# Optimization experiments

Measured on AMD Instinct MI355X. Metric: run time of the kernel, lower is better.

The kernel has to match this reference:

```python
import jax, jax.numpy as jnp
import numpy as np

B, NPTS, NBASIS, DIM, H, CH = 8, 1024, 8, 8, 512, 16
EPSILON = 1000.0
P = 2
VOLUME = 2.0 ** DIM  # MC domain [-1,1]^dim


def setup_inputs() -> dict:
    key = jax.random.key(0)
    ks = jax.random.split(key, 10)
    s = jax.random.uniform(ks[0], (NPTS, DIM), dtype=jnp.float32) * 2.0 - 1.0  # MC samples in [-1,1]^dim
    x = jax.random.uniform(ks[1], (1, DIM), dtype=jnp.float32) * 2.0 - 1.0     # eval point
    Wfirst = jax.random.normal(ks[2], (DIM, H), dtype=jnp.float32) / np.sqrt(DIM)
    bfirst = jax.random.normal(ks[3], (H,), dtype=jnp.float32) * 0.01
    Wb = jax.random.normal(ks[4], (NBASIS, H, H), dtype=jnp.float32) / np.sqrt(H)
    bb = jax.random.normal(ks[5], (NBASIS, H), dtype=jnp.float32) * 0.01
    Wlast = jax.random.normal(ks[6], (H, CH), dtype=jnp.float32) / np.sqrt(H)
    blast = jax.random.normal(ks[7], (CH,), dtype=jnp.float32) * 0.01
    Wf = jax.random.normal(ks[8], (DIM, CH), dtype=jnp.float32) / np.sqrt(DIM)
    bf = jax.random.normal(ks[9], (CH,), dtype=jnp.float32) * 0.01
    return dict(s=s, x=x, Wfirst=Wfirst, bfirst=bfirst, Wb=Wb, bb=bb,
                Wlast=Wlast, blast=blast, Wf=Wf, bf=bf)


def _basis_all(pts, Wfirst, bfirst, Wb, bb, Wlast, blast):
    # pts: [M, DIM] -> all n basis nets, batch-repeated: [NBASIS, B, M, CH]
    a0 = jax.nn.elu(jnp.einsum('md,dh->mh', pts, Wfirst) + bfirst)          # [M, H]
    a0 = jnp.broadcast_to(a0[None], (B,) + a0.shape)                         # [B, M, H] (repeat over batch)
    a1 = jax.nn.elu(jnp.einsum('bmh,ihk->ibmk', a0, Wb) + bb[:, None, None, :])  # [n, B, M, H]
    return jnp.einsum('ibmk,kc->ibmc', a1, Wlast) + blast                    # [n, B, M, CH]


def reference(s, x, Wfirst, bfirst, Wb, bb, Wlast, blast, Wf, bf):
    # func(s): linear map realizing the projected function  [NPTS, CH]
    f_s = jnp.einsum('nd,dc->nc', s, Wf) + bf
    basis_s = _basis_all(s, Wfirst, bfirst, Wb, bb, Wlast, blast)            # [n, B, NPTS, CH]
    diff = f_s[None, None] - basis_s                                          # broadcast over n, B
    # Monte Carlo integral of (func - basis_i)^p over [-1,1]^dim, per channel
    integral = VOLUME * jnp.mean(diff ** P, axis=-2)                          # [n, B, CH]
    norm_pc = integral ** (1.0 / P)                                           # Lp norm per channel
    norm_b = jnp.sum(jnp.abs(norm_pc) ** P, axis=-1, keepdims=True) ** (1.0 / P)  # [n, B, 1]
    mu = jnp.where(norm_b <= EPSILON, norm_b, 0.0)                            # [n, B, 1]
    basis_x = _basis_all(x, Wfirst, bfirst, Wb, bb, Wlast, blast)[:, :, 0, :]  # [n, B, CH]
    out = jnp.sum(mu * basis_x, axis=0)                                       # [B, CH]
    normalization = 1e-7 + jnp.sum(mu, axis=0)                                # [B, 1]
    return out / normalization
```

## Files before the change

### kernel.cpp

```cpp
#include <hip/hip_runtime.h>

typedef _Float16 half8 __attribute__((ext_vector_type(8)));
typedef float f32x4 __attribute__((ext_vector_type(4)));
typedef float f32x16 __attribute__((ext_vector_type(16)));
typedef unsigned int u32x4 __attribute__((ext_vector_type(4)));

#define NPTS 1024
#define NB 8
#define HDIM 512
#define CH 16
#define RT 1056

#define OFF_WBF 0u
#define OFF_A0F (4u*1024u*1024u)
#define A0SZ    (64u*RT*16u)
#define OFF_WLF (OFF_A0F + A0SZ)
#define OFF_FS  (OFF_WLF + 16384u)
#define OFF_IS  (OFF_FS + 65536u)
#define OFF_BX  (OFF_IS + 64u)
#define OFF_CT  (OFF_BX + 512u)

__device__ __forceinline__ float elu(float z) { return z > 0.f ? z : expm1f(z); }

__global__ __launch_bounds__(256) void kPrep(const float* __restrict__ s,
    const float* __restrict__ x, const float* __restrict__ Wfirst,
    const float* __restrict__ bfirst, const float* __restrict__ Wb,
    const float* __restrict__ Wlast, const float* __restrict__ Wf,
    const float* __restrict__ bf,
    _Float16* __restrict__ Wbf, _Float16* __restrict__ Wlf,
    _Float16* __restrict__ a0f, float* __restrict__ f_s,
    float* __restrict__ Isum, unsigned* __restrict__ cnt) {
  __shared__ __align__(16) float sm[8192];
  int b = blockIdx.x, t = threadIdx.x;
  if (b < 1024) {
    int i = b >> 7, koct = (b >> 1) & 63, n = (b & 1) * 256 + t;
    const float* src = Wb + ((size_t)i * 512 + koct * 8) * 512 + n;
    float v[8];
#pragma unroll
    for (int j = 0; j < 8; ++j) v[j] = src[j * 512];
    union { _Float16 h[8]; u32x4 u; } hu;
#pragma unroll
    for (int j = 0; j < 8; ++j) hu.h[j] = (_Float16)v[j];
    *(u32x4*)(Wbf + ((size_t)(i * 64 + koct) * 512 + n) * 8) = hu.u;
  } else if (b < 1288) {
    int rr = t >> 6, tl = t & 63;
    int m = (b - 1024) * 4 + rr;
    float* sv = &sm[rr * 8];
    if (tl < 8) sv[tl] = (m < 1024) ? s[m * 8 + tl] : (m == 1024 ? x[tl] : 0.f);
    __syncthreads();
    size_t o = ((size_t)tl * RT + m) * 8;
    if (m <= 1024) {
      float acc[8];
#pragma unroll
      for (int jj = 0; jj < 8; ++jj) acc[jj] = bfirst[8 * tl + jj];
#pragma unroll
      for (int d = 0; d < 8; ++d) {
        float sd = sv[d];
        f32x4 w0 = *(const f32x4*)&Wfirst[d * 512 + 8 * tl];
        f32x4 w1 = *(const f32x4*)&Wfirst[d * 512 + 8 * tl + 4];
#pragma unroll
        for (int e = 0; e < 4; ++e) { acc[e] += sd * w0[e]; acc[4 + e] += sd * w1[e]; }
      }
      union { _Float16 h[8]; u32x4 u; } hu;
#pragma unroll
      for (int jj = 0; jj < 8; ++jj) hu.h[jj] = (_Float16)elu(acc[jj]);
      *(u32x4*)(a0f + o) = hu.u;
      if (m < 1024 && tl < 16) {
        float a = bf[tl];
#pragma unroll
        for (int d = 0; d < 8; ++d) a += sv[d] * Wf[d * 16 + tl];
        f_s[m * 16 + tl] = a;
      }
    } else {
      u32x4 z;
#pragma unroll
      for (int e = 0; e < 4; ++e) z[e] = 0u;
      *(u32x4*)(a0f + o) = z;
    }
  } else {
    if (t < 8) Isum[t] = 0.f;
    if (t == 8) *cnt = 0u;
#pragma unroll
    for (int it = 0; it < 32; ++it) sm[t + 256 * it] = Wlast[t + 256 * it];
    __syncthreads();
#pragma unroll
    for (int p = 0; p < 4; ++p) {
      int oi = p * 256 + t;
      int ko = oi >> 4, ch = oi & 15;
      union { _Float16 h[8]; u32x4 u; } hu;
#pragma unroll
      for (int jj = 0; jj < 8; ++jj) hu.h[jj] = (_Float16)sm[(ko * 8 + jj) * 16 + ch];
      *(u32x4*)(Wlf + oi * 8) = hu.u;
    }
  }
}

__global__ __launch_bounds__(256, 2) void kB(const _Float16* __restrict__ Wbf,
    const _Float16* __restrict__ a0f, const _Float16* __restrict__ Wlf,
    const float* __restrict__ bb, const float* __restrict__ blast,
    const float* __restrict__ f_s, float* __restrict__ Isum,
    float* __restrict__ basisx, unsigned* __restrict__ cnt,
    float* __restrict__ out) {
  __shared__ u32x4 SC[512];
  __shared__ float S2[32][16];
  __shared__ float wsum[4];
  __shared__ unsigned oc;
  __shared__ float muL[8];
  int t = threadIdx.x, b = blockIdx.x;
  int i = b & 7, mt = b >> 3;
  int m0 = mt * 32;
  int w = t >> 6, lane = t & 63, ln = lane & 31, q = lane >> 5, q4 = lane >> 4;

  const u32x4* a4 = (const u32x4*)a0f;
  const u32x4* b4 = (const u32x4*)Wbf;
  int ma = m0 + ln, ib = i * 64;
  int nwl = w * 32 + ln;

  f32x16 acc[4];
#pragma unroll
  for (int j = 0; j < 4; ++j)
#pragma unroll
    for (int rr = 0; rr < 16; ++rr) acc[j][rr] = 0.f;

  u32x4 pa[3][2], pb[3][2][4];
#pragma unroll
  for (int st = 0; st < 2; ++st) {
    int k0 = st * 4 + q, k1 = k0 + 2;
    pa[st][0] = a4[k0 * RT + ma];
    pa[st][1] = a4[k1 * RT + ma];
#pragma unroll
    for (int j = 0; j < 4; ++j) {
      pb[st][0][j] = b4[(size_t)(ib + k0) * 512 + nwl + 128 * j];
      pb[st][1][j] = b4[(size_t)(ib + k1) * 512 + nwl + 128 * j];
    }
  }
#pragma unroll
  for (int ks = 0; ks < 16; ++ks) {
    int sl = ks % 3;
    if (ks < 14) {
      int sn = (ks + 2) % 3;
      int k0 = (ks + 2) * 4 + q, k1 = k0 + 2;
      pa[sn][0] = a4[k0 * RT + ma];
      pa[sn][1] = a4[k1 * RT + ma];
#pragma unroll
      for (int j = 0; j < 4; ++j) {
        pb[sn][0][j] = b4[(size_t)(ib + k0) * 512 + nwl + 128 * j];
        pb[sn][1][j] = b4[(size_t)(ib + k1) * 512 + nwl + 128 * j];
      }
    }
#pragma unroll
    for (int sfx = 0; sfx < 2; ++sfx) {
      half8 aH = __builtin_bit_cast(half8, pa[sl][sfx]);
#pragma unroll
      for (int j = 0; j < 4; ++j)
        acc[j] = __builtin_amdgcn_mfma_f32_32x32x16_f16(
            aH, __builtin_bit_cast(half8, pb[sl][sfx][j]), acc[j], 0, 0, 0);
    }
  }

  ((float*)S2)[t] = 0.f;
  ((float*)S2)[t + 256] = 0.f;
  __syncthreads();

  _Float16* scr = (_Float16*)&SC[w * 128];
  const u32x4* s4 = &SC[w * 128];
  const u32x4* w4 = (const u32x4*)Wlf;
  int ch = lane & 15;
#pragma unroll
  for (int j = 0; j < 4; ++j) {
    int nw = w * 32 + 128 * j;
    float bcol = bb[i * 512 + nw + ln];
#pragma unroll
    for (int rr = 0; rr < 16; ++rr) {
      int row = (rr & 3) + 8 * (rr >> 2) + 4 * q;
      float a1 = elu(acc[j][rr] + bcol);
      int oi = (row >> 4) * 64 + (ln >> 3) * 16 + (row & 15);
      scr[oi * 8 + (ln & 7)] = (_Float16)a1;
    }
    half8 wv = __builtin_bit_cast(half8, w4[(size_t)((nw >> 3) + q4) * 16 + ch]);
#pragma unroll
    for (int mt2 = 0; mt2 < 2; ++mt2) {
      f32x4 D2;
#pragma unroll
      for (int rr = 0; rr < 4; ++rr) D2[rr] = 0.f;
      half8 pv = __builtin_bit_cast(half8, s4[mt2 * 64 + q4 * 16 + ch]);
      D2 = __builtin_amdgcn_mfma_f32_16x16x32_f16(pv, wv, D2, 0, 0, 0);
#pragma unroll
      for (int rr = 0; rr < 4; ++rr)
        atomicAdd(&S2[mt2 * 16 + q4 * 4 + rr][ch], D2[rr]);
    }
  }
  __syncthreads();

  if (mt == 32) {
    if (t < 16) basisx[i * 16 + t] = S2[0][t] + blast[t];
  } else {
    float loc = 0.f;
#pragma unroll
    for (int p = 0; p < 2; ++p) {
      int item = t + p * 256;
      int ml = item >> 4, c2 = item & 15;
      float bs = S2[ml][c2] + blast[c2];
      float d = f_s[(size_t)(m0 + ml) * 16 + c2] - bs;
      loc += d * d;
    }
    loc += __shfl_xor(loc, 1, 64);
    loc += __shfl_xor(loc, 2, 64);
    loc += __shfl_xor(loc, 4, 64);
    loc += __shfl_xor(loc, 8, 64);
    loc += __shfl_xor(loc, 16, 64);
    loc += __shfl_xor(loc, 32, 64);
    if (lane == 0) wsum[w] = loc;
    __syncthreads();
    if (t == 0) atomicAdd(&Isum[i], wsum[0] + wsum[1] + wsum[2] + wsum[3]);
  }

  if (t == 0) {
    __threadfence();
    oc = atomicAdd(cnt, 1u);
  }
  __syncthreads();
  if (oc == 263) {
    __threadfence();
    if (t < 8) {
      float S = atomicAdd(&Isum[t], 0.f);
      float nb = 0.5f * sqrtf(S);
      muL[t] = (nb <= 1000.0f) ? nb : 0.f;
    }
    __syncthreads();
    if (t < 128) {
      int c2 = t & 15;
      float num = 0.f, den = 1e-7f;
#pragma unroll
      for (int ii = 0; ii < NB; ++ii) {
        float bx = atomicAdd(&basisx[ii * 16 + c2], 0.f);
        num += muL[ii] * bx;
        den += muL[ii];
      }
      out[t] = num / den;
    }
  }
}

extern "C" void kernel_launch(void* const* d_in, const int* in_sizes, int n_in,
                              void* d_out, int out_size, void* d_ws, size_t ws_size,
                              hipStream_t stream) {
  const float* s      = (const float*)d_in[0];
  const float* x      = (const float*)d_in[1];
  const float* Wfirst = (const float*)d_in[2];
  const float* bfirst = (const float*)d_in[3];
  const float* Wb     = (const float*)d_in[4];
  const float* bb     = (const float*)d_in[5];
  const float* Wlast  = (const float*)d_in[6];
  const float* blast  = (const float*)d_in[7];
  const float* Wf     = (const float*)d_in[8];
  const float* bf     = (const float*)d_in[9];

  char* ws = (char*)d_ws;
  _Float16* Wbf = (_Float16*)(ws + OFF_WBF);
  _Float16* a0f = (_Float16*)(ws + OFF_A0F);
  _Float16* Wlf = (_Float16*)(ws + OFF_WLF);
  float* f_s    = (float*)(ws + OFF_FS);
  float* Isum   = (float*)(ws + OFF_IS);
  float* basisx = (float*)(ws + OFF_BX);
  unsigned* cnt = (unsigned*)(ws + OFF_CT);
  float* out    = (float*)d_out;

  kPrep<<<1289, 256, 0, stream>>>(s, x, Wfirst, bfirst, Wb, Wlast, Wf, bf,
                                  Wbf, Wlf, a0f, f_s, Isum, cnt);
  kB<<<264, 256, 0, stream>>>(Wbf, a0f, Wlf, bb, blast, f_s, Isum, basisx, cnt, out);
}
```

Measured before the change: 131.2 us.

## Split kB's N dimension across 16 waves per 1024-thread block

The main kernel moves from 256 threads per block, where each wave computed four 32-column tiles, to 1024 threads per block, where each of 16 waves computes a single 32x32 tile. Per-wave accumulator and prefetch register use drops from four f32x16 accumulators to one, and the prefetch pipeline is deepened from three to four stages. The intent is more waves in flight and more latency hiding. In exchange, each wave loads the same A rows independently, shared memory per block grows, and the LDS atomics into S2 now come from 16 waves. The column reduction also fills its scratch before a barrier instead of interleaving with the ELU pass.

```diff
diff --git a/kernel.cpp b/kernel.cpp
--- a/kernel.cpp
+++ b/kernel.cpp
@@ -95,100 +95,85 @@
   }
 }
 
-__global__ __launch_bounds__(256, 2) void kB(const _Float16* __restrict__ Wbf,
+__global__ __launch_bounds__(1024, 4) void kB(const _Float16* __restrict__ Wbf,
     const _Float16* __restrict__ a0f, const _Float16* __restrict__ Wlf,
     const float* __restrict__ bb, const float* __restrict__ blast,
     const float* __restrict__ f_s, float* __restrict__ Isum,
     float* __restrict__ basisx, unsigned* __restrict__ cnt,
     float* __restrict__ out) {
-  __shared__ u32x4 SC[512];
+  __shared__ u32x4 SC[2048];
   __shared__ float S2[32][16];
-  __shared__ float wsum[4];
+  __shared__ float wsum[16];
   __shared__ unsigned oc;
   __shared__ float muL[8];
   int t = threadIdx.x, b = blockIdx.x;
   int i = b & 7, mt = b >> 3;
   int m0 = mt * 32;
   int w = t >> 6, lane = t & 63, ln = lane & 31, q = lane >> 5, q4 = lane >> 4;
+  int nw = w * 32;
 
   const u32x4* a4 = (const u32x4*)a0f;
   const u32x4* b4 = (const u32x4*)Wbf;
-  int ma = m0 + ln, ib = i * 64;
-  int nwl = w * 32 + ln;
-
-  f32x16 acc[4];
-#pragma unroll
-  for (int j = 0; j < 4; ++j)
-#pragma unroll
-    for (int rr = 0; rr < 16; ++rr) acc[j][rr] = 0.f;
-
-  u32x4 pa[3][2], pb[3][2][4];
-#pragma unroll
-  for (int st = 0; st < 2; ++st) {
+  int ma = m0 + ln, nb = nw + ln, ib = i * 64;
+
+  f32x16 acc;
+#pragma unroll
+  for (int rr = 0; rr < 16; ++rr) acc[rr] = 0.f;
+
+  u32x4 pa[4][2], pb[4][2];
+#pragma unroll
+  for (int st = 0; st < 3; ++st) {
     int k0 = st * 4 + q, k1 = k0 + 2;
     pa[st][0] = a4[k0 * RT + ma];
     pa[st][1] = a4[k1 * RT + ma];
-#pragma unroll
-    for (int j = 0; j < 4; ++j) {
-      pb[st][0][j] = b4[(size_t)(ib + k0) * 512 + nwl + 128 * j];
-      pb[st][1][j] = b4[(size_t)(ib + k1) * 512 + nwl + 128 * j];
-    }
+    pb[st][0] = b4[(size_t)(ib + k0) * 512 + nb];
+    pb[st][1] = b4[(size_t)(ib + k1) * 512 + nb];
   }
 #pragma unroll
   for (int ks = 0; ks < 16; ++ks) {
-    int sl = ks % 3;
-    if (ks < 14) {
-      int sn = (ks + 2) % 3;
-      int k0 = (ks + 2) * 4 + q, k1 = k0 + 2;
+    int sl = ks & 3;
+    acc = __builtin_amdgcn_mfma_f32_32x32x16_f16(
+        __builtin_bit_cast(half8, pa[sl][0]), __builtin_bit_cast(half8, pb[sl][0]), acc, 0, 0, 0);
+    acc = __builtin_amdgcn_mfma_f32_32x32x16_f16(
+        __builtin_bit_cast(half8, pa[sl][1]), __builtin_bit_cast(half8, pb[sl][1]), acc, 0, 0, 0);
+    if (ks < 13) {
+      int sn = (ks + 3) & 3;
+      int k0 = (ks + 3) * 4 + q, k1 = k0 + 2;
       pa[sn][0] = a4[k0 * RT + ma];
       pa[sn][1] = a4[k1 * RT + ma];
-#pragma unroll
-      for (int j = 0; j < 4; ++j) {
-        pb[sn][0][j] = b4[(size_t)(ib + k0) * 512 + nwl + 128 * j];
-        pb[sn][1][j] = b4[(size_t)(ib + k1) * 512 + nwl + 128 * j];
-      }
-    }
-#pragma unroll
-    for (int sfx = 0; sfx < 2; ++sfx) {
-      half8 aH = __builtin_bit_cast(half8, pa[sl][sfx]);
-#pragma unroll
-      for (int j = 0; j < 4; ++j)
-        acc[j] = __builtin_amdgcn_mfma_f32_32x32x16_f16(
-            aH, __builtin_bit_cast(half8, pb[sl][sfx][j]), acc[j], 0, 0, 0);
-    }
-  }
-
-  ((float*)S2)[t] = 0.f;
-  ((float*)S2)[t + 256] = 0.f;
-  __syncthreads();
-
+      pb[sn][0] = b4[(size_t)(ib + k0) * 512 + nb];
+      pb[sn][1] = b4[(size_t)(ib + k1) * 512 + nb];
+    }
+  }
+
+  if (t < 512) ((float*)S2)[t] = 0.f;
+  __syncthreads();
+
+  float bcol = bb[i * 512 + nw + ln];
   _Float16* scr = (_Float16*)&SC[w * 128];
+#pragma unroll
+  for (int rr = 0; rr < 16; ++rr) {
+    int row = (rr & 3) + 8 * (rr >> 2) + 4 * q;
+    float a1 = elu(acc[rr] + bcol);
+    int oi = (row >> 4) * 64 + (ln >> 3) * 16 + (row & 15);
+    scr[oi * 8 + (ln & 7)] = (_Float16)a1;
+  }
+  __syncthreads();
+
   const u32x4* s4 = &SC[w * 128];
   const u32x4* w4 = (const u32x4*)Wlf;
   int ch = lane & 15;
-#pragma unroll
-  for (int j = 0; j < 4; ++j) {
-    int nw = w * 32 + 128 * j;
-    float bcol = bb[i * 512 + nw + ln];
-#pragma unroll
-    for (int rr = 0; rr < 16; ++rr) {
-      int row = (rr & 3) + 8 * (rr >> 2) + 4 * q;
-      float a1 = elu(acc[j][rr] + bcol);
-      int oi = (row >> 4) * 64 + (ln >> 3) * 16 + (row & 15);
-      scr[oi * 8 + (ln & 7)] = (_Float16)a1;
-    }
-    half8 wv = __builtin_bit_cast(half8, w4[(size_t)((nw >> 3) + q4) * 16 + ch]);
-#pragma unroll
-    for (int mt2 = 0; mt2 < 2; ++mt2) {
-      f32x4 D2;
-#pragma unroll
-      for (int rr = 0; rr < 4; ++rr) D2[rr] = 0.f;
-      half8 pv = __builtin_bit_cast(half8, s4[mt2 * 64 + q4 * 16 + ch]);
-      D2 = __builtin_amdgcn_mfma_f32_16x16x32_f16(pv, wv, D2, 0, 0, 0);
-#pragma unroll
-      for (int rr = 0; rr < 4; ++rr)
-        atomicAdd(&S2[mt2 * 16 + q4 * 4 + rr][ch], D2[rr]);
-    }
+  half8 wv = __builtin_bit_cast(half8, w4[(size_t)((nw >> 3) + q4) * 16 + ch]);
+#pragma unroll
+  for (int mt2 = 0; mt2 < 2; ++mt2) {
+    f32x4 D2;
+#pragma unroll
+    for (int rr = 0; rr < 4; ++rr) D2[rr] = 0.f;
+    half8 pv = __builtin_bit_cast(half8, s4[mt2 * 64 + q4 * 16 + ch]);
+    D2 = __builtin_amdgcn_mfma_f32_16x16x32_f16(pv, wv, D2, 0, 0, 0);
+#pragma unroll
+    for (int rr = 0; rr < 4; ++rr)
+      atomicAdd(&S2[mt2 * 16 + q4 * 4 + rr][ch], D2[rr]);
   }
   __syncthreads();
 
@@ -196,13 +181,11 @@
     if (t < 16) basisx[i * 16 + t] = S2[0][t] + blast[t];
   } else {
     float loc = 0.f;
-#pragma unroll
-    for (int p = 0; p < 2; ++p) {
-      int item = t + p * 256;
-      int ml = item >> 4, c2 = item & 15;
+    if (t < 512) {
+      int ml = t >> 4, c2 = t & 15;
       float bs = S2[ml][c2] + blast[c2];
       float d = f_s[(size_t)(m0 + ml) * 16 + c2] - bs;
-      loc += d * d;
+      loc = d * d;
     }
     loc += __shfl_xor(loc, 1, 64);
     loc += __shfl_xor(loc, 2, 64);
@@ -212,7 +195,12 @@
     loc += __shfl_xor(loc, 32, 64);
     if (lane == 0) wsum[w] = loc;
     __syncthreads();
-    if (t == 0) atomicAdd(&Isum[i], wsum[0] + wsum[1] + wsum[2] + wsum[3]);
+    if (t == 0) {
+      float S = 0.f;
+#pragma unroll
+      for (int ww = 0; ww < 16; ++ww) S += wsum[ww];
+      atomicAdd(&Isum[i], S);
+    }
   }
 
   if (t == 0) {
@@ -268,5 +256,5 @@
 
   kPrep<<<1289, 256, 0, stream>>>(s, x, Wfirst, bfirst, Wb, Wlast, Wf, bf,
                                   Wbf, Wlf, a0f, f_s, Isum, cnt);
-  kB<<<264, 256, 0, stream>>>(Wbf, a0f, Wlf, bb, blast, f_s, Isum, basisx, cnt, out);
+  kB<<<264, 1024, 0, stream>>>(Wbf, a0f, Wlf, bb, blast, f_s, Isum, basisx, cnt, out);
 }
```

Measured after the change: 126.6 us. -3.5%, faster.
